# Optimization experiments

Hardware: AMD Instinct MI355X
Metric: run time of the kernel (lower is better)

The kernel has to match this reference:

```python
import jax, jax.numpy as jnp
import numpy as np

B, DIN, H, DOUT = 4096, 2048, 4096, 2048


def setup_inputs() -> dict:
    key = jax.random.key(0)
    ks = jax.random.split(key, 17)
    x = jax.random.normal(ks[0], (B, DIN), dtype=jnp.float32)
    W0 = jax.random.randint(ks[1], (H, DIN), -127, 128, dtype=jnp.int32)
    b0 = jax.random.randint(ks[2], (H,), -127, 128, dtype=jnp.int32)
    W2 = jax.random.randint(ks[3], (H, H), -127, 128, dtype=jnp.int32)
    b2 = jax.random.randint(ks[4], (H,), -127, 128, dtype=jnp.int32)
    W4 = jax.random.randint(ks[5], (DOUT, H), -127, 128, dtype=jnp.int32)
    b4 = jax.random.randint(ks[6], (DOUT,), -127, 128, dtype=jnp.int32)
    # amax scalars: positive calibration ranges in [0.5, 2.0)
    amaxes = [jax.random.uniform(ks[7 + i], (), jnp.float32, 0.5, 2.0) for i in range(9)]
    (a0_in, a0_w, a0_b, a2_in, a2_w, a2_b, a4_in, a4_w, a4_b) = amaxes
    return {"x": x, "W0": W0, "b0": b0, "W2": W2, "b2": b2, "W4": W4, "b4": b4,
            "a0_in": a0_in, "a0_w": a0_w, "a0_b": a0_b,
            "a2_in": a2_in, "a2_w": a2_w, "a2_b": a2_b,
            "a4_in": a4_in, "a4_w": a4_w, "a4_b": a4_b}


def _quant(x, amax):
    # torch: clamp(round(x * 127/amax), -127, 127).int()
    scale = 127.0 / amax
    return jnp.clip(jnp.round(x * scale), -127.0, 127.0).astype(jnp.int32)


def _layer(x, W, b, a_in, a_w, a_b):
    xq = _quant(x, a_in)                                      # [B, in] int32
    acc = jnp.matmul(xq, W.T, preferred_element_type=jnp.int32)  # [B, out] int32
    y = acc.astype(jnp.float32) * (a_w * a_in / (127.0 ** 2))    # double dequant
    return y + b.astype(jnp.float32) * (a_b / 127.0)             # single dequant bias


def reference(x, W0, b0, W2, b2, W4, b4,
              a0_in, a0_w, a0_b, a2_in, a2_w, a2_b, a4_in, a4_w, a4_b):
    x = x.reshape(x.shape[0], -1)
    x = _layer(x, W0, b0, a0_in, a0_w, a0_b)
    x = jax.nn.relu(x)
    x = _layer(x, W2, b2, a2_in, a2_w, a2_b)
    x = jax.nn.relu(x)
    x = _layer(x, W4, b4, a4_in, a4_w, a4_b)
    return x
```

## Files before the change

### kernel.cpp

```cpp
#include <hip/hip_runtime.h>

using i32x4 = __attribute__((ext_vector_type(4))) int;

#define DEVI static __device__ __forceinline__

DEVI void gload_lds16(const void* g, void* l) {
  __builtin_amdgcn_global_load_lds(
      (const __attribute__((address_space(1))) void*)g,
      (__attribute__((address_space(3))) void*)l, 16, 0, 0);
}

template <int N> DEVI void vmcnt_n() {
  asm volatile("s_waitcnt vmcnt(%0)" ::"n"(N) : "memory");
}
template <int N> DEVI void lgkm_n() {
  asm volatile("s_waitcnt lgkmcnt(%0)" ::"n"(N) : "memory");
}

#define FENCE() asm volatile("" ::: "memory")
#define BARX()                    \
  do {                            \
    FENCE();                      \
    __builtin_amdgcn_s_barrier(); \
    FENCE();                      \
  } while (0)
#define SCHB() __builtin_amdgcn_sched_barrier(0)
#define PRIO1() __builtin_amdgcn_s_setprio(1)
#define PRIO0() __builtin_amdgcn_s_setprio(0)

__global__ void __launch_bounds__(256) pack_w_kernel(const int* __restrict__ w,
                                                     signed char* __restrict__ o,
                                                     int n4) {
  int stride = gridDim.x * blockDim.x;
  for (int i = blockIdx.x * blockDim.x + threadIdx.x; i < n4; i += stride) {
    int4 v = reinterpret_cast<const int4*>(w)[i];
    char4 c;
    c.x = (signed char)v.x;
    c.y = (signed char)v.y;
    c.z = (signed char)v.z;
    c.w = (signed char)v.w;
    reinterpret_cast<char4*>(o)[i] = c;
  }
}

__global__ void __launch_bounds__(256) quant_x_kernel(const float* __restrict__ x,
                                                      signed char* __restrict__ o,
                                                      const float* __restrict__ amax,
                                                      int n4) {
  const float s = 127.0f / amax[0];
  int stride = gridDim.x * blockDim.x;
  for (int i = blockIdx.x * blockDim.x + threadIdx.x; i < n4; i += stride) {
    float4 v = reinterpret_cast<const float4*>(x)[i];
    char4 c;
    float q;
    q = fminf(fmaxf(rintf(__fmul_rn(v.x, s)), -127.0f), 127.0f); c.x = (signed char)(int)q;
    q = fminf(fmaxf(rintf(__fmul_rn(v.y, s)), -127.0f), 127.0f); c.y = (signed char)(int)q;
    q = fminf(fmaxf(rintf(__fmul_rn(v.z, s)), -127.0f), 127.0f); c.z = (signed char)(int)q;
    q = fminf(fmaxf(rintf(__fmul_rn(v.w, s)), -127.0f), 127.0f); c.w = (signed char)(int)q;
    reinterpret_cast<char4*>(o)[i] = c;
  }
}


#define GB(b, j, k0_)                                           \
  gload_lds16(Wb + (size_t)((j)*64 + srow) * K + (k0_),         \
              &lds[b][ABYTES + (j)*8192 + tid * 16])
#define GA(b, r0, k0_)                                          \
  gload_lds16(Ab + (size_t)((r0) + srow) * K + (k0_),           \
              &lds[b][(r0)*128 + tid * 16])

#define STG_B(b, kt)                               \
  do {                                             \
    const int k0_ = (kt)*128 + scol;               \
    _Pragma("unroll") for (int j = 0; j < NN; ++j) GB(b, j, k0_); \
  } while (0)
#define STG_A(b, kt)                 \
  do {                               \
    const int k0_ = (kt)*128 + scol; \
    GA(b, 0, k0_);                   \
    GA(b, 128, k0_);                 \
    GA(b, 64, k0_);                  \
    GA(b, 192, k0_);                 \
  } while (0)

#define AF_(b, m, h) \
  (*(const i32x4*)&lds[b][(wrl + (m)*16 + ro) * 128 + ((h) ? cS1 : cS0)])
#define BF_(b, n, h) \
  (*(const i32x4*)&lds[b][ABYTES + (wcl + (n)*16 + ro) * 128 + ((h) ? cS1 : cS0)])

#define RD_AF(dst, b, m0)          \
  do {                             \
    dst[0][0] = AF_(b, m0, 0);     \
    dst[0][1] = AF_(b, m0, 1);     \
    dst[1][0] = AF_(b, (m0) + 1, 0); \
    dst[1][1] = AF_(b, (m0) + 1, 1); \
  } while (0)

#define READ_BF(b)                                   \
  do {                                               \
    _Pragma("unroll") for (int n = 0; n < NN; ++n) { \
      bf[n][0] = BF_(b, n, 0);                       \
      bf[n][1] = BF_(b, n, 1);                       \
    }                                                \
  } while (0)

#define MFMA_P(mp, af)                                                                     \
  do {                                                                                     \
    _Pragma("unroll") for (int n = 0; n < NN; ++n) {                                       \
      acc[2 * (mp)][n] =                                                                   \
          __builtin_amdgcn_mfma_i32_16x16x64_i8(af[0][0], bf[n][0], acc[2 * (mp)][n], 0, 0, 0); \
      acc[2 * (mp)][n] =                                                                   \
          __builtin_amdgcn_mfma_i32_16x16x64_i8(af[0][1], bf[n][1], acc[2 * (mp)][n], 0, 0, 0); \
      acc[2 * (mp) + 1][n] = __builtin_amdgcn_mfma_i32_16x16x64_i8(                        \
          af[1][0], bf[n][0], acc[2 * (mp) + 1][n], 0, 0, 0);                              \
      acc[2 * (mp) + 1][n] = __builtin_amdgcn_mfma_i32_16x16x64_i8(                        \
          af[1][1], bf[n][1], acc[2 * (mp) + 1][n], 0, 0, 0);                              \
    }                                                                                      \
  } while (0)

#define TILE_STEADY(b, t)                       \
  do {                                          \
    READ_BF(b);                                 \
    RD_AF(afB, b, 2);                           \
    STG_B(1 - (b), (t) + 1);                    \
    vmcnt_n<VM0>();                             \
    BARX(); lgkm_n<4>(); SCHB();                \
    PRIO1(); MFMA_P(0, afA); PRIO0();           \
    RD_AF(afA, b, 4);                           \
    STG_A(1 - (b), (t) + 1);                    \
    BARX(); lgkm_n<4>(); SCHB();                \
    PRIO1(); MFMA_P(1, afB); PRIO0();           \
    RD_AF(afB, b, 6);                           \
    vmcnt_n<2>();                               \
    BARX(); lgkm_n<4>(); SCHB();                \
    PRIO1(); MFMA_P(2, afA); PRIO0();           \
    RD_AF(afA, 1 - (b), 0);                     \
    BARX(); lgkm_n<4>(); SCHB();                \
    PRIO1(); MFMA_P(3, afB); PRIO0();           \
  } while (0)

#define TILE_LAST(b)                            \
  do {                                          \
    READ_BF(b);                                 \
    RD_AF(afB, b, 2);                           \
    vmcnt_n<0>();                               \
    BARX(); lgkm_n<4>(); SCHB();                \
    PRIO1(); MFMA_P(0, afA); PRIO0();           \
    RD_AF(afA, b, 4);                           \
    BARX(); lgkm_n<4>(); SCHB();                \
    PRIO1(); MFMA_P(1, afB); PRIO0();           \
    RD_AF(afB, b, 6);                           \
    BARX(); lgkm_n<4>(); SCHB();                \
    PRIO1(); MFMA_P(2, afA); PRIO0();           \
    BARX(); lgkm_n<0>(); SCHB();                \
    PRIO1(); MFMA_P(3, afB); PRIO0();           \
  } while (0)

template <int BN, int OUT_I8>
__global__ __launch_bounds__(512, 2) void gemm8_kernel(
    const signed char* __restrict__ A, const signed char* __restrict__ W,
    const int* __restrict__ bias, void* __restrict__ out, int M, int N, int K,
    const float* __restrict__ p_ain, const float* __restrict__ p_aw,
    const float* __restrict__ p_ab, const float* __restrict__ p_anext) {
  static_assert(BN == 256 || BN == 128, "");
  constexpr int NN = BN / 64;
  constexpr int VM0 = (NN == 4) ? 4 : 2;
  constexpr int ABYTES = 256 * 128;
  __shared__ signed char lds[2][ABYTES + BN * 128];

  const int tid = threadIdx.x;
  const int lane = tid & 63;
  const int wave = tid >> 6;
  const int wrl = (wave >> 2) * 128;
  const int wcl = (wave & 3) * (BN / 4);
  const int tileM = blockIdx.y * 256;
  const int tileN = blockIdx.x * BN;

  const signed char* Ab = A + (size_t)tileM * K;
  const signed char* Wb = W + (size_t)tileN * K;

  const int srow = tid >> 3;
  const int scol = ((tid & 7) ^ (srow & 7)) * 16;

  const int ro = lane & 15;
  const int kg = lane >> 4;
  const int cS0 = ((kg ^ (ro & 7)) << 4);
  const int cS1 = (((4 + kg) ^ (ro & 7)) << 4);

  const int nt = K >> 7;

  i32x4 acc[8][NN] = {};
  i32x4 afA[2][2], afB[2][2], bf[NN][2];

  STG_B(0, 0);
  STG_A(0, 0);
  vmcnt_n<2>();
  BARX();
  RD_AF(afA, 0, 0);

  for (int t = 0; t < nt - 2; t += 2) {
    TILE_STEADY(0, t);
    TILE_STEADY(1, t + 1);
  }
  TILE_STEADY(0, nt - 2);
  TILE_LAST(1);

  const float s1 = __fmul_rn(p_aw[0], p_ain[0]) / 16129.0f;
  const float s2 = p_ab[0] / 127.0f;
  float qs = 0.0f;
  if (OUT_I8) qs = 127.0f / p_anext[0];

#pragma unroll
  for (int m = 0; m < 8; ++m) {
#pragma unroll
    for (int n = 0; n < NN; ++n) {
      const int col = tileN + wcl + n * 16 + ro;
      const int row0 = tileM + wrl + m * 16 + kg * 4;
      const float bv = __fmul_rn((float)bias[col], s2);
#pragma unroll
      for (int i = 0; i < 4; ++i) {
        float y = __fadd_rn(__fmul_rn((float)acc[m][n][i], s1), bv);
        if (OUT_I8) {
          float rl = fmaxf(y, 0.0f);
          float q = fminf(rintf(__fmul_rn(rl, qs)), 127.0f);
          ((signed char*)out)[(size_t)(row0 + i) * N + col] = (signed char)(int)q;
        } else {
          ((float*)out)[(size_t)(row0 + i) * N + col] = y;
        }
      }
    }
  }
}

extern "C" void kernel_launch(void* const* d_in, const int* in_sizes, int n_in,
                              void* d_out, int out_size, void* d_ws, size_t ws_size,
                              hipStream_t stream) {
  const float* x = (const float*)d_in[0];
  const int* W0 = (const int*)d_in[1];
  const int* b0 = (const int*)d_in[2];
  const int* W2 = (const int*)d_in[3];
  const int* b2 = (const int*)d_in[4];
  const int* W4 = (const int*)d_in[5];
  const int* b4 = (const int*)d_in[6];
  const float* a0_in = (const float*)d_in[7];
  const float* a0_w = (const float*)d_in[8];
  const float* a0_b = (const float*)d_in[9];
  const float* a2_in = (const float*)d_in[10];
  const float* a2_w = (const float*)d_in[11];
  const float* a2_b = (const float*)d_in[12];
  const float* a4_in = (const float*)d_in[13];
  const float* a4_w = (const float*)d_in[14];
  const float* a4_b = (const float*)d_in[15];

  constexpr int Bb = 4096, DIN = 2048, H = 4096, DOUT = 2048;
  constexpr size_t MB = 1u << 20;

  char* ws = (char*)d_ws;
  signed char* xq0 = (signed char*)(ws);
  signed char* xq2 = (signed char*)(ws);
  signed char* W0q = (signed char*)(ws + 8 * MB);
  signed char* W2q = (signed char*)(ws + 16 * MB);
  signed char* W4q = (signed char*)(ws + 32 * MB);
  signed char* xq1 = (signed char*)(ws + 40 * MB);

  pack_w_kernel<<<2048, 256, 0, stream>>>(W0, W0q, H * DIN / 4);
  pack_w_kernel<<<2048, 256, 0, stream>>>(W2, W2q, H * H / 4);
  pack_w_kernel<<<2048, 256, 0, stream>>>(W4, W4q, DOUT * H / 4);
  quant_x_kernel<<<2048, 256, 0, stream>>>(x, xq0, a0_in, Bb * DIN / 4);

  gemm8_kernel<256, 1><<<dim3(H / 256, Bb / 256), 512, 0, stream>>>(
      xq0, W0q, b0, xq1, Bb, H, DIN, a0_in, a0_w, a0_b, a2_in);
  gemm8_kernel<256, 1><<<dim3(H / 256, Bb / 256), 512, 0, stream>>>(
      xq1, W2q, b2, xq2, Bb, H, H, a2_in, a2_w, a2_b, a4_in);
  gemm8_kernel<128, 0><<<dim3(DOUT / 128, Bb / 256), 512, 0, stream>>>(
      xq2, W4q, b4, d_out, Bb, DOUT, H, a4_in, a4_w, a4_b, a4_in);
}
```

Measured before the change: 171.5 us.

## Split B-tile prefetch so half is issued a tile earlier

The B-tile global-to-LDS loads are split into an early half and a late half. The early half is issued during the previous tile's last MFMA phase, which gives those loads more time in flight before they are needed. The A loads are also split into two pairs spread across phases, and the vmcnt waits are adjusted to match. This reworks the cross-phase load schedule and relies on the buffer being free once RD_AF of the other buffer has been issued, which adds a risk of an LDS race if the barriers do not cover it.

Result: faster. 166.4 us (-3.0%).

```diff
diff --git a/kernel.cpp b/kernel.cpp
--- a/kernel.cpp
+++ b/kernel.cpp
@@ -69,16 +69,25 @@
   gload_lds16(Ab + (size_t)((r0) + srow) * K + (k0_),           \
               &lds[b][(r0)*128 + tid * 16])
 
-#define STG_B(b, kt)                               \
-  do {                                             \
-    const int k0_ = (kt)*128 + scol;               \
-    _Pragma("unroll") for (int j = 0; j < NN; ++j) GB(b, j, k0_); \
-  } while (0)
-#define STG_A(b, kt)                 \
+#define STG_B_EARLY(b, kt)                                              \
+  do {                                                                  \
+    const int k0_ = (kt)*128 + scol;                                    \
+    _Pragma("unroll") for (int j = 0; j < NBE; ++j) GB(b, j, k0_);      \
+  } while (0)
+#define STG_B_LATE(b, kt)                                               \
+  do {                                                                  \
+    const int k0_ = (kt)*128 + scol;                                    \
+    _Pragma("unroll") for (int j = NBE; j < NN; ++j) GB(b, j, k0_);     \
+  } while (0)
+#define STG_A01(b, kt)               \
   do {                               \
     const int k0_ = (kt)*128 + scol; \
     GA(b, 0, k0_);                   \
     GA(b, 128, k0_);                 \
+  } while (0)
+#define STG_A23(b, kt)               \
+  do {                               \
+    const int k0_ = (kt)*128 + scol; \
     GA(b, 64, k0_);                  \
     GA(b, 192, k0_);                 \
   } while (0)
@@ -88,10 +97,10 @@
 #define BF_(b, n, h) \
   (*(const i32x4*)&lds[b][ABYTES + (wcl + (n)*16 + ro) * 128 + ((h) ? cS1 : cS0)])
 
-#define RD_AF(dst, b, m0)          \
-  do {                             \
-    dst[0][0] = AF_(b, m0, 0);     \
-    dst[0][1] = AF_(b, m0, 1);     \
+#define RD_AF(dst, b, m0)            \
+  do {                               \
+    dst[0][0] = AF_(b, m0, 0);       \
+    dst[0][1] = AF_(b, m0, 1);       \
     dst[1][0] = AF_(b, (m0) + 1, 0); \
     dst[1][1] = AF_(b, (m0) + 1, 1); \
   } while (0)
@@ -122,12 +131,13 @@
   do {                                          \
     READ_BF(b);                                 \
     RD_AF(afB, b, 2);                           \
-    STG_B(1 - (b), (t) + 1);                    \
-    vmcnt_n<VM0>();                             \
+    STG_B_LATE(1 - (b), (t) + 1);               \
+    STG_A01(1 - (b), (t) + 1);                  \
+    vmcnt_n<NN + 2>();                          \
     BARX(); lgkm_n<4>(); SCHB();                \
     PRIO1(); MFMA_P(0, afA); PRIO0();           \
     RD_AF(afA, b, 4);                           \
-    STG_A(1 - (b), (t) + 1);                    \
+    STG_A23(1 - (b), (t) + 1);                  \
     BARX(); lgkm_n<4>(); SCHB();                \
     PRIO1(); MFMA_P(1, afB); PRIO0();           \
     RD_AF(afB, b, 6);                           \
@@ -135,6 +145,7 @@
     BARX(); lgkm_n<4>(); SCHB();                \
     PRIO1(); MFMA_P(2, afA); PRIO0();           \
     RD_AF(afA, 1 - (b), 0);                     \
+    if ((t) + 2 < nt) STG_B_EARLY(b, (t) + 2);  \
     BARX(); lgkm_n<4>(); SCHB();                \
     PRIO1(); MFMA_P(3, afB); PRIO0();           \
   } while (0)
@@ -164,7 +175,7 @@
     const float* __restrict__ p_ab, const float* __restrict__ p_anext) {
   static_assert(BN == 256 || BN == 128, "");
   constexpr int NN = BN / 64;
-  constexpr int VM0 = (NN == 4) ? 4 : 2;
+  constexpr int NBE = NN / 2;
   constexpr int ABYTES = 256 * 128;
   __shared__ signed char lds[2][ABYTES + BN * 128];
 
@@ -192,9 +203,18 @@
   i32x4 acc[8][NN] = {};
   i32x4 afA[2][2], afB[2][2], bf[NN][2];
 
-  STG_B(0, 0);
-  STG_A(0, 0);
-  vmcnt_n<2>();
+  {
+    const int k0_ = scol;
+#pragma unroll
+    for (int j = 0; j < NN; ++j) GB(0, j, k0_);
+    GA(0, 0, k0_);
+    GA(0, 128, k0_);
+    GA(0, 64, k0_);
+    GA(0, 192, k0_);
+  }
+  FENCE();
+  STG_B_EARLY(1, 1);
+  vmcnt_n<NBE>();
   BARX();
   RD_AF(afA, 0, 0);
 
```

## Load A fragments directly from global memory and swizzle tile order for locality

Applied to the files above, without the earlier changes.

A tiles are no longer staged through LDS. Each wave loads its A fragments straight from global memory into registers, so LDS holds only the double-buffered W tile. The main loop is restructured so there are fewer barriers per K step, and a block-index swizzle groups tiles across 8 partitions (likely XCDs) to improve L2 reuse. The cost is that A loads now go directly to global memory without LDS sharing, and waves in the same row re-read the same A data, which raises L2 traffic and exposes load latency.

Result: slower. 377.6 us (+120.2%).

```diff
diff --git a/kernel.cpp b/kernel.cpp
--- a/kernel.cpp
+++ b/kernel.cpp
@@ -62,39 +62,16 @@
 }
 
 
-#define GB(b, j, k0_)                                           \
-  gload_lds16(Wb + (size_t)((j)*64 + srow) * K + (k0_),         \
-              &lds[b][ABYTES + (j)*8192 + tid * 16])
-#define GA(b, r0, k0_)                                          \
-  gload_lds16(Ab + (size_t)((r0) + srow) * K + (k0_),           \
-              &lds[b][(r0)*128 + tid * 16])
-
-#define STG_B(b, kt)                               \
-  do {                                             \
-    const int k0_ = (kt)*128 + scol;               \
-    _Pragma("unroll") for (int j = 0; j < NN; ++j) GB(b, j, k0_); \
-  } while (0)
-#define STG_A(b, kt)                 \
-  do {                               \
-    const int k0_ = (kt)*128 + scol; \
-    GA(b, 0, k0_);                   \
-    GA(b, 128, k0_);                 \
-    GA(b, 64, k0_);                  \
-    GA(b, 192, k0_);                 \
-  } while (0)
-
-#define AF_(b, m, h) \
-  (*(const i32x4*)&lds[b][(wrl + (m)*16 + ro) * 128 + ((h) ? cS1 : cS0)])
+#define STG(b, kt)                                                       \
+  do {                                                                   \
+    const int k0_ = (kt)*128 + scol;                                     \
+    _Pragma("unroll") for (int j = 0; j < NN; ++j)                       \
+        gload_lds16(Wb + (size_t)((j)*64 + srow) * K + k0_,              \
+                    &lds[b][(j)*8192 + tid * 16]);                       \
+  } while (0)
+
 #define BF_(b, n, h) \
-  (*(const i32x4*)&lds[b][ABYTES + (wcl + (n)*16 + ro) * 128 + ((h) ? cS1 : cS0)])
-
-#define RD_AF(dst, b, m0)          \
-  do {                             \
-    dst[0][0] = AF_(b, m0, 0);     \
-    dst[0][1] = AF_(b, m0, 1);     \
-    dst[1][0] = AF_(b, (m0) + 1, 0); \
-    dst[1][1] = AF_(b, (m0) + 1, 1); \
-  } while (0)
+  (*(const i32x4*)&lds[b][(wcl + (n)*16 + ro) * 128 + ((h) ? cS1 : cS0)])
 
 #define READ_BF(b)                                   \
   do {                                               \
@@ -102,6 +79,14 @@
       bf[n][0] = BF_(b, n, 0);                       \
       bf[n][1] = BF_(b, n, 1);                       \
     }                                                \
+  } while (0)
+
+#define LD_AF(dst, mp, kb)                                                  \
+  do {                                                                      \
+    dst[0][0] = *(const i32x4*)(Gp + (size_t)(2 * (mp)) * MS + (kb));       \
+    dst[0][1] = *(const i32x4*)(Gp + (size_t)(2 * (mp)) * MS + (kb) + 64);  \
+    dst[1][0] = *(const i32x4*)(Gp + (size_t)(2 * (mp) + 1) * MS + (kb));   \
+    dst[1][1] = *(const i32x4*)(Gp + (size_t)(2 * (mp) + 1) * MS + (kb) + 64); \
   } while (0)
 
 #define MFMA_P(mp, af)                                                                     \
@@ -118,63 +103,46 @@
     }                                                                                      \
   } while (0)
 
-#define TILE_STEADY(b, t)                       \
-  do {                                          \
-    READ_BF(b);                                 \
-    RD_AF(afB, b, 2);                           \
-    STG_B(1 - (b), (t) + 1);                    \
-    vmcnt_n<VM0>();                             \
-    BARX(); lgkm_n<4>(); SCHB();                \
-    PRIO1(); MFMA_P(0, afA); PRIO0();           \
-    RD_AF(afA, b, 4);                           \
-    STG_A(1 - (b), (t) + 1);                    \
-    BARX(); lgkm_n<4>(); SCHB();                \
-    PRIO1(); MFMA_P(1, afB); PRIO0();           \
-    RD_AF(afB, b, 6);                           \
-    vmcnt_n<2>();                               \
-    BARX(); lgkm_n<4>(); SCHB();                \
-    PRIO1(); MFMA_P(2, afA); PRIO0();           \
-    RD_AF(afA, 1 - (b), 0);                     \
-    BARX(); lgkm_n<4>(); SCHB();                \
-    PRIO1(); MFMA_P(3, afB); PRIO0();           \
-  } while (0)
-
-#define TILE_LAST(b)                            \
-  do {                                          \
-    READ_BF(b);                                 \
-    RD_AF(afB, b, 2);                           \
-    vmcnt_n<0>();                               \
-    BARX(); lgkm_n<4>(); SCHB();                \
-    PRIO1(); MFMA_P(0, afA); PRIO0();           \
-    RD_AF(afA, b, 4);                           \
-    BARX(); lgkm_n<4>(); SCHB();                \
-    PRIO1(); MFMA_P(1, afB); PRIO0();           \
-    RD_AF(afB, b, 6);                           \
-    BARX(); lgkm_n<4>(); SCHB();                \
-    PRIO1(); MFMA_P(2, afA); PRIO0();           \
-    BARX(); lgkm_n<0>(); SCHB();                \
-    PRIO1(); MFMA_P(3, afB); PRIO0();           \
+#define TILE_R7(b, t)                              \
+  do {                                             \
+    const int kb = (t)*128;                        \
+    const int tn = ((t) + 1 < nt) ? (t) + 1 : (t); \
+    READ_BF(b);                                    \
+    STG(1 - (b), tn);                              \
+    lgkm_n<0>(); SCHB();                           \
+    PRIO1(); MFMA_P(0, af0); PRIO0();              \
+    LD_AF(af0, 2, kb);                             \
+    PRIO1(); MFMA_P(1, af1); PRIO0();              \
+    LD_AF(af1, 3, kb);                             \
+    PRIO1(); MFMA_P(2, af0); PRIO0();              \
+    PRIO1(); MFMA_P(3, af1); PRIO0();              \
+    vmcnt_n<0>();                                  \
+    LD_AF(af0, 0, tn * 128);                       \
+    LD_AF(af1, 1, tn * 128);                       \
+    BARX();                                        \
   } while (0)
 
 template <int BN, int OUT_I8>
-__global__ __launch_bounds__(512, 2) void gemm8_kernel(
+__global__ __launch_bounds__(512, 2) void gemm_r7_kernel(
     const signed char* __restrict__ A, const signed char* __restrict__ W,
     const int* __restrict__ bias, void* __restrict__ out, int M, int N, int K,
     const float* __restrict__ p_ain, const float* __restrict__ p_aw,
     const float* __restrict__ p_ab, const float* __restrict__ p_anext) {
   static_assert(BN == 256 || BN == 128, "");
   constexpr int NN = BN / 64;
-  constexpr int VM0 = (NN == 4) ? 4 : 2;
-  constexpr int ABYTES = 256 * 128;
-  __shared__ signed char lds[2][ABYTES + BN * 128];
+  __shared__ signed char lds[2][BN * 128];
 
   const int tid = threadIdx.x;
   const int lane = tid & 63;
   const int wave = tid >> 6;
   const int wrl = (wave >> 2) * 128;
   const int wcl = (wave & 3) * (BN / 4);
-  const int tileM = blockIdx.y * 256;
-  const int tileN = blockIdx.x * BN;
+
+  const int lin = blockIdx.y * gridDim.x + blockIdx.x;
+  const int cpx = (gridDim.x * gridDim.y) >> 3;
+  const int swz = (lin & 7) * cpx + (lin >> 3);
+  const int tileM = (swz / gridDim.x) * 256;
+  const int tileN = (swz % gridDim.x) * BN;
 
   const signed char* Ab = A + (size_t)tileM * K;
   const signed char* Wb = W + (size_t)tileN * K;
@@ -187,23 +155,25 @@
   const int cS0 = ((kg ^ (ro & 7)) << 4);
   const int cS1 = (((4 + kg) ^ (ro & 7)) << 4);
 
+  const size_t MS = (size_t)16 * K;
+  const signed char* Gp = Ab + (size_t)(wrl + ro) * K + kg * 16;
+
   const int nt = K >> 7;
 
   i32x4 acc[8][NN] = {};
-  i32x4 afA[2][2], afB[2][2], bf[NN][2];
-
-  STG_B(0, 0);
-  STG_A(0, 0);
-  vmcnt_n<2>();
+  i32x4 af0[2][2], af1[2][2], bf[NN][2];
+
+  STG(0, 0);
+  vmcnt_n<0>();
+  LD_AF(af0, 0, 0);
+  LD_AF(af1, 1, 0);
   BARX();
-  RD_AF(afA, 0, 0);
-
-  for (int t = 0; t < nt - 2; t += 2) {
-    TILE_STEADY(0, t);
-    TILE_STEADY(1, t + 1);
-  }
-  TILE_STEADY(0, nt - 2);
-  TILE_LAST(1);
+
+  for (int t = 0; t < nt; t += 2) {
+    TILE_R7(0, t);
+    TILE_R7(1, t + 1);
+  }
+  vmcnt_n<0>();
 
   const float s1 = __fmul_rn(p_aw[0], p_ain[0]) / 16129.0f;
   const float s2 = p_ab[0] / 127.0f;
@@ -268,10 +238,10 @@
   pack_w_kernel<<<2048, 256, 0, stream>>>(W4, W4q, DOUT * H / 4);
   quant_x_kernel<<<2048, 256, 0, stream>>>(x, xq0, a0_in, Bb * DIN / 4);
 
-  gemm8_kernel<256, 1><<<dim3(H / 256, Bb / 256), 512, 0, stream>>>(
+  gemm_r7_kernel<256, 1><<<dim3(H / 256, Bb / 256), 512, 0, stream>>>(
       xq0, W0q, b0, xq1, Bb, H, DIN, a0_in, a0_w, a0_b, a2_in);
-  gemm8_kernel<256, 1><<<dim3(H / 256, Bb / 256), 512, 0, stream>>>(
+  gemm_r7_kernel<256, 1><<<dim3(H / 256, Bb / 256), 512, 0, stream>>>(
       xq1, W2q, b2, xq2, Bb, H, H, a2_in, a2_w, a2_b, a4_in);
-  gemm8_kernel<128, 0><<<dim3(DOUT / 128, Bb / 256), 512, 0, stream>>>(
+  gemm_r7_kernel<128, 0><<<dim3(DOUT / 128, Bb / 256), 512, 0, stream>>>(
       xq2, W4q, b4, d_out, Bb, DOUT, H, a4_in, a4_w, a4_b, a4_in);
 }
```
